# Performance work log

Hardware: AMD Instinct MI355X
Metric: run time of the kernel (lower is better)

Reference implementation:

```python
import jax, jax.numpy as jnp
import numpy as np

NEG_INF = -1e9  # mask fill; every row has >=1 valid key so softmax is well-defined


def setup_inputs() -> dict:
    B, L, E, A = 4096, 200, 128, 128
    key = jax.random.key(0)
    ks = jax.random.split(key, 8)
    scale = 0.05
    return {
        "query": jax.random.normal(ks[0], (B, E), dtype=jnp.float32),
        "keys": jax.random.normal(ks[1], (B, L, E), dtype=jnp.float32),
        "keys_length": jax.random.randint(ks[2], (B,), 1, L + 1, dtype=jnp.int64),
        "pos_emb": jax.random.normal(ks[3], (L, E), dtype=jnp.float32) * scale,
        "W1": jax.random.normal(ks[4], (4 * E, A), dtype=jnp.float32) * scale,
        "b1": jnp.zeros((A,), dtype=jnp.float32),
        "W2": jax.random.normal(ks[5], (A, A), dtype=jnp.float32) * scale,
        "b2": jnp.zeros((A,), dtype=jnp.float32),
        "W3": jax.random.normal(ks[6], (A, 1), dtype=jnp.float32) * scale,
        "b3": jnp.zeros((1,), dtype=jnp.float32),
    }


def reference(query, keys, keys_length, pos_emb, W1, b1, W2, b2, W3, b3):
    B, L, E = keys.shape
    # add position embedding (positions are simply arange(L) for every batch row)
    keys_p = keys + pos_emb[None, :, :]                      # (B, L, E)
    q = jnp.broadcast_to(query[:, None, :], (B, L, E))       # (B, L, E)
    # DIN attention input: [q, k, q-k, q*k] -> (B, L, 4E)
    att_in = jnp.concatenate([q, keys_p, q - keys_p, q * keys_p], axis=-1)
    h = jax.nn.relu(att_in @ W1 + b1)                        # (B, L, A)
    h = jax.nn.relu(h @ W2 + b2)                             # (B, L, A)
    scores = (h @ W3 + b3)[..., 0]                           # (B, L)
    valid = jnp.arange(L)[None, :] < keys_length[:, None]    # (B, L) bool
    scores = jnp.where(valid, scores, NEG_INF)
    weights = jax.nn.softmax(scores, axis=-1)                # (B, L)
    out = jnp.einsum("bl,ble->be", weights, keys_p)          # (B, E)
    return out
```

## Files before the change

kernel.cpp:

```cpp
#include <hip/hip_runtime.h>
#include <hip/hip_bf16.h>


typedef __attribute__((ext_vector_type(8))) short short8;
typedef __attribute__((ext_vector_type(4))) float f32x4;

__device__ __forceinline__ float bf2f(short s) {
    return __uint_as_float(((unsigned)(unsigned short)s) << 16);
}
__device__ __forceinline__ short f2bf(float f) {
    unsigned u = __float_as_uint(f);
    u = (u + 0x7fff + ((u >> 16) & 1)) >> 16;
    return (short)u;
}

__global__ void prep_w(const float* __restrict__ W1, const float* __restrict__ W2,
                       short* __restrict__ wkT, short* __restrict__ wqkT,
                       short* __restrict__ w2T) {
    int i = blockIdx.x * 256 + threadIdx.x;
    int k = i >> 7, n = i & 127;
    wkT [n * 128 + k] = f2bf(W1[(128 + k) * 128 + n] - W1[(256 + k) * 128 + n]);
    wqkT[n * 128 + k] = f2bf(W1[(384 + k) * 128 + n]);
    w2T [n * 128 + k] = f2bf(W2[k * 128 + n]);
}

__global__ void prep_qw(const float* __restrict__ query, const float* __restrict__ W1,
                        const float* __restrict__ b1, float* __restrict__ qw) {
    __shared__ float qsh[128];
    const int b = blockIdx.x, t = threadIdx.x;
    qsh[t] = query[b * 128 + t];
    __syncthreads();
    float acc = b1[t];
    #pragma unroll 4
    for (int k = 0; k < 128; ++k)
        acc += qsh[k] * (W1[k * 128 + t] + W1[(256 + k) * 128 + t]);
    qw[b * 128 + t] = acc;
}

#define STR 136

__launch_bounds__(256, 1)
__global__ void din_main(const float* __restrict__ query, const float* __restrict__ keys,
                         const int* __restrict__ klen, const float* __restrict__ pos,
                         const float* __restrict__ b2g, const float* __restrict__ w3g,
                         const float* __restrict__ qw, const short* __restrict__ wkT,
                         const short* __restrict__ wqkT, const short* __restrict__ w2Tg,
                         float* __restrict__ out) {
    __shared__ alignas(16) short kp[208 * STR];
    __shared__ alignas(16) short w1eff[128 * STR];
    __shared__ alignas(16) short w2t[128 * STR];
    __shared__ alignas(16) short h1s[4 * 16 * STR];
    __shared__ float qv[128];
    __shared__ float s_lds[208];
    __shared__ float w_lds[208];
    __shared__ float part[4 * 128];
    __shared__ float red[8];

    const int t = threadIdx.x;
    const int b = blockIdx.x;
    const int w = t >> 6;
    const int lane = t & 63;
    const int quad = lane >> 4;
    const int l15 = lane & 15;

    if (t < 128) qv[t] = query[b * 128 + t];
    __syncthreads();

    for (int i = t; i < 8192; i += 256) {
        int n = i >> 6, kk = (i & 63) * 2;
        unsigned a = *(const unsigned*)(wkT + n * 128 + kk);
        unsigned c = *(const unsigned*)(wqkT + n * 128 + kk);
        float v0 = bf2f((short)(a & 0xffff)) + qv[kk]     * bf2f((short)(c & 0xffff));
        float v1 = bf2f((short)(a >> 16))    + qv[kk + 1] * bf2f((short)(c >> 16));
        *(unsigned*)(w1eff + n * STR + kk) =
            (unsigned)(unsigned short)f2bf(v0) | ((unsigned)(unsigned short)f2bf(v1) << 16);
    }
    for (int i = t; i < 2048; i += 256) {
        int n = i >> 4, seg = (i & 15) * 8;
        *(short8*)(w2t + n * STR + seg) = *(const short8*)(w2Tg + n * 128 + seg);
    }

    float qwn[8], b2n[8], w3n[8];
    #pragma unroll
    for (int n = 0; n < 8; ++n) {
        qwn[n] = qw[b * 128 + n * 16 + l15];
        b2n[n] = b2g[n * 16 + l15];
        w3n[n] = w3g[n * 16 + l15];
    }
    __syncthreads();

    short* h1w = h1s + w * 16 * STR;

    for (int tile = w; tile < 13; tile += 4) {
        #pragma unroll
        for (int i = 0; i < 4; ++i) {
            int row = quad + 4 * i;
            int l = tile * 16 + row;
            short8 kp8;
            if (l < 200) {
                const float4* kr = (const float4*)(keys + ((long)b * 200 + l) * 128);
                const float4* pr = (const float4*)(pos + (long)l * 128);
                float4 k0 = kr[l15 * 2], k1 = kr[l15 * 2 + 1];
                float4 p0 = pr[l15 * 2], p1 = pr[l15 * 2 + 1];
                kp8[0] = f2bf(k0.x + p0.x); kp8[1] = f2bf(k0.y + p0.y);
                kp8[2] = f2bf(k0.z + p0.z); kp8[3] = f2bf(k0.w + p0.w);
                kp8[4] = f2bf(k1.x + p1.x); kp8[5] = f2bf(k1.y + p1.y);
                kp8[6] = f2bf(k1.z + p1.z); kp8[7] = f2bf(k1.w + p1.w);
            } else {
                #pragma unroll
                for (int j = 0; j < 8; ++j) kp8[j] = 0;
            }
            *(short8*)(kp + (tile * 16 + row) * STR + l15 * 8) = kp8;
        }

        f32x4 acc[8];
        #pragma unroll
        for (int n = 0; n < 8; ++n) acc[n] = (f32x4){0.f, 0.f, 0.f, 0.f};
        #pragma unroll
        for (int s = 0; s < 4; ++s) {
            short8 a = *(const short8*)(kp + (tile * 16 + l15) * STR + s * 32 + quad * 8);
            #pragma unroll
            for (int n = 0; n < 8; ++n) {
                short8 bb = *(const short8*)(w1eff + (n * 16 + l15) * STR + s * 32 + quad * 8);
                acc[n] = __builtin_amdgcn_mfma_f32_16x16x32_bf16(a, bb, acc[n], 0, 0, 0);
            }
        }
        #pragma unroll
        for (int n = 0; n < 8; ++n) {
            #pragma unroll
            for (int r = 0; r < 4; ++r) {
                float v = acc[n][r] + qwn[n];
                h1w[(quad * 4 + r) * STR + n * 16 + l15] = f2bf(v > 0.f ? v : 0.f);
            }
        }
        #pragma unroll
        for (int n = 0; n < 8; ++n) acc[n] = (f32x4){0.f, 0.f, 0.f, 0.f};
        #pragma unroll
        for (int s = 0; s < 4; ++s) {
            short8 a = *(const short8*)(h1w + l15 * STR + s * 32 + quad * 8);
            #pragma unroll
            for (int n = 0; n < 8; ++n) {
                short8 bb = *(const short8*)(w2t + (n * 16 + l15) * STR + s * 32 + quad * 8);
                acc[n] = __builtin_amdgcn_mfma_f32_16x16x32_bf16(a, bb, acc[n], 0, 0, 0);
            }
        }
        float p[4] = {0.f, 0.f, 0.f, 0.f};
        #pragma unroll
        for (int n = 0; n < 8; ++n) {
            #pragma unroll
            for (int r = 0; r < 4; ++r) {
                float v = acc[n][r] + b2n[n];
                p[r] += (v > 0.f ? v : 0.f) * w3n[n];
            }
        }
        #pragma unroll
        for (int off = 8; off >= 1; off >>= 1) {
            #pragma unroll
            for (int r = 0; r < 4; ++r) p[r] += __shfl_xor(p[r], off, 64);
        }
        if (l15 == 0) {
            #pragma unroll
            for (int r = 0; r < 4; ++r) s_lds[tile * 16 + quad * 4 + r] = p[r];
        }
    }
    __syncthreads();

    const int len = klen[b];
    float sv = (t < 208 && t < len) ? s_lds[t] : -1e9f;
    float m = sv;
    #pragma unroll
    for (int off = 32; off >= 1; off >>= 1) m = fmaxf(m, __shfl_xor(m, off, 64));
    if (lane == 0) red[w] = m;
    __syncthreads();
    m = fmaxf(fmaxf(red[0], red[1]), fmaxf(red[2], red[3]));
    float e = (t < 208) ? expf(sv - m) : 0.f;
    float ssum = e;
    #pragma unroll
    for (int off = 32; off >= 1; off >>= 1) ssum += __shfl_xor(ssum, off, 64);
    if (lane == 0) red[4 + w] = ssum;
    __syncthreads();
    float S = red[4] + red[5] + red[6] + red[7];
    if (t < 208) w_lds[t] = e / S;
    __syncthreads();

    const int qt = t >> 6;
    const int e2 = (t & 63) * 2;
    float ax = 0.f, ay = 0.f;
    for (int l = qt * 52; l < qt * 52 + 52; ++l) {
        float wgt = w_lds[l];
        unsigned pr = *(const unsigned*)(kp + l * STR + e2);
        ax += wgt * __uint_as_float(pr << 16);
        ay += wgt * __uint_as_float(pr & 0xffff0000u);
    }
    part[qt * 128 + e2] = ax;
    part[qt * 128 + e2 + 1] = ay;
    __syncthreads();
    if (t < 128) {
        float o = part[t] + part[128 + t] + part[256 + t] + part[384 + t];
        out[b * 128 + t] = o;
    }
}

extern "C" void kernel_launch(void* const* d_in, const int* in_sizes, int n_in,
                              void* d_out, int out_size, void* d_ws, size_t ws_size,
                              hipStream_t stream) {
    const float* query = (const float*)d_in[0];
    const float* keys  = (const float*)d_in[1];
    const int*   klen  = (const int*)  d_in[2];
    const float* pos   = (const float*)d_in[3];
    const float* W1    = (const float*)d_in[4];
    const float* b1    = (const float*)d_in[5];
    const float* W2    = (const float*)d_in[6];
    const float* b2    = (const float*)d_in[7];
    const float* W3    = (const float*)d_in[8];
    float* out = (float*)d_out;

    char* ws = (char*)d_ws;
    float* qw   = (float*)ws;
    short* wkT  = (short*)(ws + 2097152);
    short* wqkT = (short*)(ws + 2097152 + 32768);
    short* w2T  = (short*)(ws + 2097152 + 65536);

    prep_w  <<<64,   256, 0, stream>>>(W1, W2, wkT, wqkT, w2T);
    prep_qw <<<4096, 128, 0, stream>>>(query, W1, b1, qw);
    din_main<<<4096, 256, 0, stream>>>(query, keys, klen, pos, b2, W3, qw,
                                       wkT, wqkT, w2T, out);
}
```

Before: 811.7 us.

## Skip masked key tiles, use pre-swizzled weight fragments, register-resident A operands

Weights are pre-arranged into MFMA fragment order in global memory so each lane loads its B fragments directly, instead of building per-block LDS copies of W1eff and W2. The q*k term is moved onto the A operand (k times q elementwise) rather than folded into a per-batch weight matrix. Only tiles up to keys_length are computed, and the final weighted sum rereads keys and pos from global for valid rows only. Dropping the large LDS buffers allows two blocks per CU. The cost is extra global/L2 traffic for weight fragments and the rereads of keys, plus more register pressure from holding four tiles of accumulators.

```diff
diff --git a/kernel.cpp b/kernel.cpp
--- a/kernel.cpp
+++ b/kernel.cpp
@@ -14,14 +14,34 @@
     return (short)u;
 }
 
-__global__ void prep_w(const float* __restrict__ W1, const float* __restrict__ W2,
-                       short* __restrict__ wkT, short* __restrict__ wqkT,
-                       short* __restrict__ w2T) {
-    int i = blockIdx.x * 256 + threadIdx.x;
-    int k = i >> 7, n = i & 127;
-    wkT [n * 128 + k] = f2bf(W1[(128 + k) * 128 + n] - W1[(256 + k) * 128 + n]);
-    wqkT[n * 128 + k] = f2bf(W1[(384 + k) * 128 + n]);
-    w2T [n * 128 + k] = f2bf(W2[k * 128 + n]);
+__global__ void prep_frag(const float* __restrict__ W1, const float* __restrict__ W2,
+                          short* __restrict__ F1, short* __restrict__ F2) {
+    int idx = blockIdx.x * 256 + threadIdx.x;
+    if (idx < 4096) {
+        int lane = idx & 63, n = (idx >> 6) & 7, kb = idx >> 9;
+        int q = lane >> 4, l15 = lane & 15;
+        int sp = kb >> 1, half = kb & 1;
+        int col = n * 16 + l15;
+        short8 v;
+        #pragma unroll
+        for (int j = 0; j < 8; ++j) {
+            int k = 32 * sp + 8 * q + j;
+            float x = half ? W1[(384 + k) * 128 + col]
+                           : W1[(128 + k) * 128 + col] - W1[(256 + k) * 128 + col];
+            v[j] = f2bf(x);
+        }
+        *(short8*)(F1 + idx * 8) = v;
+    } else if (idx < 6144) {
+        int i2 = idx - 4096;
+        int lane = i2 & 63, n = (i2 >> 6) & 7, s2 = i2 >> 9;
+        int q = lane >> 4, l15 = lane & 15;
+        int col = n * 16 + l15;
+        short8 v;
+        #pragma unroll
+        for (int j = 0; j < 8; ++j)
+            v[j] = f2bf(W2[(32 * s2 + 8 * q + j) * 128 + col]);
+        *(short8*)(F2 + i2 * 8) = v;
+    }
 }
 
 __global__ void prep_qw(const float* __restrict__ query, const float* __restrict__ W1,
@@ -37,23 +57,19 @@
     qw[b * 128 + t] = acc;
 }
 
-#define STR 136
-
-__launch_bounds__(256, 1)
+#define HSTR 136
+
+__launch_bounds__(256, 2)
 __global__ void din_main(const float* __restrict__ query, const float* __restrict__ keys,
                          const int* __restrict__ klen, const float* __restrict__ pos,
                          const float* __restrict__ b2g, const float* __restrict__ w3g,
-                         const float* __restrict__ qw, const short* __restrict__ wkT,
-                         const short* __restrict__ wqkT, const short* __restrict__ w2Tg,
-                         float* __restrict__ out) {
-    __shared__ alignas(16) short kp[208 * STR];
-    __shared__ alignas(16) short w1eff[128 * STR];
-    __shared__ alignas(16) short w2t[128 * STR];
-    __shared__ alignas(16) short h1s[4 * 16 * STR];
+                         const float* __restrict__ qw, const short* __restrict__ F1,
+                         const short* __restrict__ F2, float* __restrict__ out) {
+    __shared__ alignas(16) short h1buf[16 * 16 * HSTR];
     __shared__ float qv[128];
     __shared__ float s_lds[208];
     __shared__ float w_lds[208];
-    __shared__ float part[4 * 128];
+    __shared__ float part[512];
     __shared__ float red[8];
 
     const int t = threadIdx.x;
@@ -63,109 +79,142 @@
     const int quad = lane >> 4;
     const int l15 = lane & 15;
 
+    const int len = klen[b];
+    const int T = (len + 15) >> 4;
+    const int cnt = (T > w) ? ((T - w + 3) >> 2) : 0;
+
     if (t < 128) qv[t] = query[b * 128 + t];
     __syncthreads();
 
-    for (int i = t; i < 8192; i += 256) {
-        int n = i >> 6, kk = (i & 63) * 2;
-        unsigned a = *(const unsigned*)(wkT + n * 128 + kk);
-        unsigned c = *(const unsigned*)(wqkT + n * 128 + kk);
-        float v0 = bf2f((short)(a & 0xffff)) + qv[kk]     * bf2f((short)(c & 0xffff));
-        float v1 = bf2f((short)(a >> 16))    + qv[kk + 1] * bf2f((short)(c >> 16));
-        *(unsigned*)(w1eff + n * STR + kk) =
-            (unsigned)(unsigned short)f2bf(v0) | ((unsigned)(unsigned short)f2bf(v1) << 16);
-    }
-    for (int i = t; i < 2048; i += 256) {
-        int n = i >> 4, seg = (i & 15) * 8;
-        *(short8*)(w2t + n * STR + seg) = *(const short8*)(w2Tg + n * 128 + seg);
-    }
-
-    float qwn[8], b2n[8], w3n[8];
+    f32x4 acc[4][8];
     #pragma unroll
-    for (int n = 0; n < 8; ++n) {
-        qwn[n] = qw[b * 128 + n * 16 + l15];
-        b2n[n] = b2g[n * 16 + l15];
-        w3n[n] = w3g[n * 16 + l15];
-    }
-    __syncthreads();
-
-    short* h1w = h1s + w * 16 * STR;
-
-    for (int tile = w; tile < 13; tile += 4) {
-        #pragma unroll
-        for (int i = 0; i < 4; ++i) {
-            int row = quad + 4 * i;
-            int l = tile * 16 + row;
-            short8 kp8;
-            if (l < 200) {
-                const float4* kr = (const float4*)(keys + ((long)b * 200 + l) * 128);
-                const float4* pr = (const float4*)(pos + (long)l * 128);
-                float4 k0 = kr[l15 * 2], k1 = kr[l15 * 2 + 1];
-                float4 p0 = pr[l15 * 2], p1 = pr[l15 * 2 + 1];
-                kp8[0] = f2bf(k0.x + p0.x); kp8[1] = f2bf(k0.y + p0.y);
-                kp8[2] = f2bf(k0.z + p0.z); kp8[3] = f2bf(k0.w + p0.w);
-                kp8[4] = f2bf(k1.x + p1.x); kp8[5] = f2bf(k1.y + p1.y);
-                kp8[6] = f2bf(k1.z + p1.z); kp8[7] = f2bf(k1.w + p1.w);
-            } else {
-                #pragma unroll
-                for (int j = 0; j < 8; ++j) kp8[j] = 0;
-            }
-            *(short8*)(kp + (tile * 16 + row) * STR + l15 * 8) = kp8;
-        }
-
-        f32x4 acc[8];
-        #pragma unroll
-        for (int n = 0; n < 8; ++n) acc[n] = (f32x4){0.f, 0.f, 0.f, 0.f};
-        #pragma unroll
-        for (int s = 0; s < 4; ++s) {
-            short8 a = *(const short8*)(kp + (tile * 16 + l15) * STR + s * 32 + quad * 8);
+    for (int i = 0; i < 4; ++i)
+        #pragma unroll
+        for (int n = 0; n < 8; ++n) acc[i][n] = (f32x4){0.f, 0.f, 0.f, 0.f};
+
+    if (cnt > 0) {
+        for (int sp = 0; sp < 4; ++sp) {
+            float4 qa = *(const float4*)(qv + 32 * sp + 8 * quad);
+            float4 qb = *(const float4*)(qv + 32 * sp + 8 * quad + 4);
+            short8 bf[8];
+            #pragma unroll
+            for (int n = 0; n < 8; ++n)
+                bf[n] = *(const short8*)(F1 + (((2 * sp) * 8 + n) * 64 + lane) * 8);
+            short8 af[4];
+            #pragma unroll
+            for (int i = 0; i < 4; ++i) {
+                if (i < cnt) {
+                    int row = (w + 4 * i) * 16 + l15;
+                    short8 a;
+                    if (row < 200) {
+                        const float* kr = keys + ((long)b * 200 + row) * 128 + 32 * sp + 8 * quad;
+                        const float* pr = pos + (long)row * 128 + 32 * sp + 8 * quad;
+                        float4 k0 = *(const float4*)kr, k1 = *(const float4*)(kr + 4);
+                        float4 p0 = *(const float4*)pr, p1 = *(const float4*)(pr + 4);
+                        a[0] = f2bf(k0.x + p0.x); a[1] = f2bf(k0.y + p0.y);
+                        a[2] = f2bf(k0.z + p0.z); a[3] = f2bf(k0.w + p0.w);
+                        a[4] = f2bf(k1.x + p1.x); a[5] = f2bf(k1.y + p1.y);
+                        a[6] = f2bf(k1.z + p1.z); a[7] = f2bf(k1.w + p1.w);
+                    } else {
+                        #pragma unroll
+                        for (int j = 0; j < 8; ++j) a[j] = 0;
+                    }
+                    af[i] = a;
+                    #pragma unroll
+                    for (int n = 0; n < 8; ++n)
+                        acc[i][n] = __builtin_amdgcn_mfma_f32_16x16x32_bf16(a, bf[n], acc[i][n], 0, 0, 0);
+                }
+            }
+            #pragma unroll
+            for (int n = 0; n < 8; ++n)
+                bf[n] = *(const short8*)(F1 + (((2 * sp + 1) * 8 + n) * 64 + lane) * 8);
+            #pragma unroll
+            for (int i = 0; i < 4; ++i) {
+                if (i < cnt) {
+                    short8 a;
+                    a[0] = f2bf(bf2f(af[i][0]) * qa.x); a[1] = f2bf(bf2f(af[i][1]) * qa.y);
+                    a[2] = f2bf(bf2f(af[i][2]) * qa.z); a[3] = f2bf(bf2f(af[i][3]) * qa.w);
+                    a[4] = f2bf(bf2f(af[i][4]) * qb.x); a[5] = f2bf(bf2f(af[i][5]) * qb.y);
+                    a[6] = f2bf(bf2f(af[i][6]) * qb.z); a[7] = f2bf(bf2f(af[i][7]) * qb.w);
+                    #pragma unroll
+                    for (int n = 0; n < 8; ++n)
+                        acc[i][n] = __builtin_amdgcn_mfma_f32_16x16x32_bf16(a, bf[n], acc[i][n], 0, 0, 0);
+                }
+            }
+        }
+
+        {
+            float qwn[8];
+            #pragma unroll
+            for (int n = 0; n < 8; ++n) qwn[n] = qw[b * 128 + n * 16 + l15];
+            #pragma unroll
+            for (int i = 0; i < 4; ++i) {
+                if (i < cnt) {
+                    #pragma unroll
+                    for (int n = 0; n < 8; ++n)
+                        #pragma unroll
+                        for (int r = 0; r < 4; ++r) {
+                            float v = acc[i][n][r] + qwn[n];
+                            h1buf[((w * 4 + i) * 16 + quad * 4 + r) * HSTR + n * 16 + l15] =
+                                f2bf(v > 0.f ? v : 0.f);
+                        }
+                }
+            }
+        }
+
+        #pragma unroll
+        for (int i = 0; i < 4; ++i)
+            #pragma unroll
+            for (int n = 0; n < 8; ++n) acc[i][n] = (f32x4){0.f, 0.f, 0.f, 0.f};
+        for (int s2 = 0; s2 < 4; ++s2) {
+            short8 bf[8];
+            #pragma unroll
+            for (int n = 0; n < 8; ++n)
+                bf[n] = *(const short8*)(F2 + ((s2 * 8 + n) * 64 + lane) * 8);
+            #pragma unroll
+            for (int i = 0; i < 4; ++i) {
+                if (i < cnt) {
+                    short8 a = *(const short8*)(h1buf + ((w * 4 + i) * 16 + l15) * HSTR + 32 * s2 + 8 * quad);
+                    #pragma unroll
+                    for (int n = 0; n < 8; ++n)
+                        acc[i][n] = __builtin_amdgcn_mfma_f32_16x16x32_bf16(a, bf[n], acc[i][n], 0, 0, 0);
+                }
+            }
+        }
+
+        {
+            float b2n[8], w3n[8];
             #pragma unroll
             for (int n = 0; n < 8; ++n) {
-                short8 bb = *(const short8*)(w1eff + (n * 16 + l15) * STR + s * 32 + quad * 8);
-                acc[n] = __builtin_amdgcn_mfma_f32_16x16x32_bf16(a, bb, acc[n], 0, 0, 0);
-            }
-        }
-        #pragma unroll
-        for (int n = 0; n < 8; ++n) {
-            #pragma unroll
-            for (int r = 0; r < 4; ++r) {
-                float v = acc[n][r] + qwn[n];
-                h1w[(quad * 4 + r) * STR + n * 16 + l15] = f2bf(v > 0.f ? v : 0.f);
-            }
-        }
-        #pragma unroll
-        for (int n = 0; n < 8; ++n) acc[n] = (f32x4){0.f, 0.f, 0.f, 0.f};
-        #pragma unroll
-        for (int s = 0; s < 4; ++s) {
-            short8 a = *(const short8*)(h1w + l15 * STR + s * 32 + quad * 8);
-            #pragma unroll
-            for (int n = 0; n < 8; ++n) {
-                short8 bb = *(const short8*)(w2t + (n * 16 + l15) * STR + s * 32 + quad * 8);
-                acc[n] = __builtin_amdgcn_mfma_f32_16x16x32_bf16(a, bb, acc[n], 0, 0, 0);
-            }
-        }
-        float p[4] = {0.f, 0.f, 0.f, 0.f};
-        #pragma unroll
-        for (int n = 0; n < 8; ++n) {
-            #pragma unroll
-            for (int r = 0; r < 4; ++r) {
-                float v = acc[n][r] + b2n[n];
-                p[r] += (v > 0.f ? v : 0.f) * w3n[n];
-            }
-        }
-        #pragma unroll
-        for (int off = 8; off >= 1; off >>= 1) {
-            #pragma unroll
-            for (int r = 0; r < 4; ++r) p[r] += __shfl_xor(p[r], off, 64);
-        }
-        if (l15 == 0) {
-            #pragma unroll
-            for (int r = 0; r < 4; ++r) s_lds[tile * 16 + quad * 4 + r] = p[r];
-        }
-    }
-    __syncthreads();
-
-    const int len = klen[b];
+                b2n[n] = b2g[n * 16 + l15];
+                w3n[n] = w3g[n * 16 + l15];
+            }
+            #pragma unroll
+            for (int i = 0; i < 4; ++i) {
+                if (i < cnt) {
+                    float p[4] = {0.f, 0.f, 0.f, 0.f};
+                    #pragma unroll
+                    for (int n = 0; n < 8; ++n)
+                        #pragma unroll
+                        for (int r = 0; r < 4; ++r) {
+                            float v = acc[i][n][r] + b2n[n];
+                            p[r] += (v > 0.f ? v : 0.f) * w3n[n];
+                        }
+                    #pragma unroll
+                    for (int off = 8; off >= 1; off >>= 1)
+                        #pragma unroll
+                        for (int r = 0; r < 4; ++r) p[r] += __shfl_xor(p[r], off, 64);
+                    if (l15 == 0) {
+                        #pragma unroll
+                        for (int r = 0; r < 4; ++r)
+                            s_lds[(w + 4 * i) * 16 + quad * 4 + r] = p[r];
+                    }
+                }
+            }
+        }
+    }
+    __syncthreads();
+
     float sv = (t < 208 && t < len) ? s_lds[t] : -1e9f;
     float m = sv;
     #pragma unroll
@@ -173,7 +222,7 @@
     if (lane == 0) red[w] = m;
     __syncthreads();
     m = fmaxf(fmaxf(red[0], red[1]), fmaxf(red[2], red[3]));
-    float e = (t < 208) ? expf(sv - m) : 0.f;
+    float e = (t < 208 && t < len) ? expf(sv - m) : 0.f;
     float ssum = e;
     #pragma unroll
     for (int off = 32; off >= 1; off >>= 1) ssum += __shfl_xor(ssum, off, 64);
@@ -184,16 +233,19 @@
     __syncthreads();
 
     const int qt = t >> 6;
-    const int e2 = (t & 63) * 2;
+    const int e2h = t & 63;
     float ax = 0.f, ay = 0.f;
-    for (int l = qt * 52; l < qt * 52 + 52; ++l) {
+    const float2* kr = (const float2*)(keys + (long)b * 200 * 128);
+    const float2* pr = (const float2*)pos;
+    for (int l = qt; l < len; l += 4) {
         float wgt = w_lds[l];
-        unsigned pr = *(const unsigned*)(kp + l * STR + e2);
-        ax += wgt * __uint_as_float(pr << 16);
-        ay += wgt * __uint_as_float(pr & 0xffff0000u);
-    }
-    part[qt * 128 + e2] = ax;
-    part[qt * 128 + e2 + 1] = ay;
+        float2 kv = kr[l * 64 + e2h];
+        float2 pv = pr[l * 64 + e2h];
+        ax += wgt * (kv.x + pv.x);
+        ay += wgt * (kv.y + pv.y);
+    }
+    part[qt * 128 + 2 * e2h]     = ax;
+    part[qt * 128 + 2 * e2h + 1] = ay;
     __syncthreads();
     if (t < 128) {
         float o = part[t] + part[128 + t] + part[256 + t] + part[384 + t];
@@ -216,13 +268,12 @@
     float* out = (float*)d_out;
 
     char* ws = (char*)d_ws;
-    float* qw   = (float*)ws;
-    short* wkT  = (short*)(ws + 2097152);
-    short* wqkT = (short*)(ws + 2097152 + 32768);
-    short* w2T  = (short*)(ws + 2097152 + 65536);
-
-    prep_w  <<<64,   256, 0, stream>>>(W1, W2, wkT, wqkT, w2T);
-    prep_qw <<<4096, 128, 0, stream>>>(query, W1, b1, qw);
-    din_main<<<4096, 256, 0, stream>>>(query, keys, klen, pos, b2, W3, qw,
-                                       wkT, wqkT, w2T, out);
-}
+    float* qw = (float*)ws;
+    short* F1 = (short*)(ws + 2097152);
+    short* F2 = (short*)(ws + 2097152 + 65536);
+
+    prep_frag<<<24,   256, 0, stream>>>(W1, W2, F1, F2);
+    prep_qw  <<<4096, 128, 0, stream>>>(query, W1, b1, qw);
+    din_main <<<4096, 256, 0, stream>>>(query, keys, klen, pos, b2, W3, qw,
+                                        F1, F2, out);
+}
```

Measured after the change: 715.7 us. 1.13x faster.
